# Kernel optimization log

Measured on AMD Instinct MI355X. Metric: run time of the kernel, lower is better.

## Reference

```python
import jax, jax.numpy as jnp
import numpy as np

NUM_STAB = 0.001  # numerical_stabilizer from relu_kernel_transformation


def relu_kernel(data, proj):
    """ReLU random-feature kernel: data [B,L,H,D], proj [M,D] -> [B,L,H,M]."""
    ratio = 1.0 / jnp.sqrt(jnp.asarray(proj.shape[0], jnp.float32))
    data_dash = ratio * jnp.einsum('blhd,md->blhm', data, proj)
    return jax.nn.relu(data_dash) + NUM_STAB


def setup_inputs() -> dict:
    key = jax.random.key(0)
    k1, k2, k3, k4 = jax.random.split(key, 4)
    B, L, H, D, M = 2, 4096, 8, 64, 256
    return {
        'query': jax.random.normal(k1, (B, L, H, D), jnp.float32),
        'key_t': jax.random.normal(k2, (B, L, H, D), jnp.float32),
        'value': jax.random.normal(k3, (B, L, H, D), jnp.float32),
        'projection_matrix': jax.random.normal(k4, (M, D), jnp.float32),
    }


def reference(query, key_t, value, projection_matrix):
    # Kernel feature maps [B,L,H,M]
    qp = relu_kernel(query, projection_matrix)
    kp = relu_kernel(key_t, projection_matrix)
    # Causal path operates in [L,B,H,*] layout
    qs = jnp.transpose(qp, (1, 0, 2, 3))     # [L,B,H,M]
    ks = jnp.transpose(kp, (1, 0, 2, 3))     # [L,B,H,M]
    vs = jnp.transpose(value, (1, 0, 2, 3))  # [L,B,H,D]

    B, H, M = qs.shape[1], qs.shape[2], qs.shape[3]
    D = vs.shape[3]
    init = (jnp.zeros((B, H, M, D), qs.dtype),  # running sum of k outer v
            jnp.zeros((B, H, M), qs.dtype))     # running sum of k

    def step(carry, inp):
        kv_sum, k_sum = carry
        q, k, v = inp  # [B,H,M], [B,H,M], [B,H,D]
        kv_sum = kv_sum + k[..., None] * v[..., None, :]
        k_sum = k_sum + k
        num = jnp.einsum('bhmd,bhm->bhd', kv_sum, q)  # causal numerator step
        den = jnp.einsum('bhm,bhm->bh', q, k_sum)     # causal denominator step
        return (kv_sum, k_sum), (num, den)

    _, (num, den) = jax.lax.scan(step, init, (qs, ks, vs))  # num [L,B,H,D], den [L,B,H]
    den = den[..., None]
    den = jnp.where(den <= 0.0, jnp.ones_like(den), den)
    out = num / den                      # [L,B,H,D]
    return jnp.transpose(out, (1, 0, 2, 3))  # [B,L,H,D]
```

## Files before the change

kernel.cpp:

```cpp
#include <hip/hip_runtime.h>
#include <hip/hip_bf16.h>


#define B_   2
#define L_   4096
#define H_   8
#define D_   64
#define M_   256
#define T_   128
#define C_   (L_ / T_)
#define NBH  (B_ * H_)
#define RATIO 0.0625f
#define STAB  0.001f
#define SVT  136
#define SQS  72

typedef __attribute__((ext_vector_type(8))) short short8;
typedef __attribute__((ext_vector_type(4))) float floatx4;

#define MFMA16(a, b, c) __builtin_amdgcn_mfma_f32_16x16x32_bf16(a, b, c, 0, 0, 0)

__device__ inline unsigned short f2bf(float x) {
    union { float f; unsigned u; } v; v.f = x;
    unsigned r = v.u + 0x7FFF + ((v.u >> 16) & 1);
    return (unsigned short)(r >> 16);
}
__device__ inline unsigned pack2bf(float a, float b) {
    __hip_bfloat162 h = __float22bfloat162_rn(make_float2(a, b));
    unsigned u; __builtin_memcpy(&u, &h, 4);
    return u;
}
__device__ inline short8 ldg8_bfs(const float* p) {
    float4 a = *(const float4*)p;
    float4 b = *(const float4*)(p + 4);
    short8 r;
    r[0] = (short)f2bf(a.x * RATIO); r[1] = (short)f2bf(a.y * RATIO);
    r[2] = (short)f2bf(a.z * RATIO); r[3] = (short)f2bf(a.w * RATIO);
    r[4] = (short)f2bf(b.x * RATIO); r[5] = (short)f2bf(b.y * RATIO);
    r[6] = (short)f2bf(b.z * RATIO); r[7] = (short)f2bf(b.w * RATIO);
    return r;
}

__global__ __launch_bounds__(256, 2)
void prep_kernel(const float* __restrict__ key, const float* __restrict__ val,
                 const float* __restrict__ proj,
                 unsigned short* __restrict__ kbf, unsigned short* __restrict__ VTg,
                 unsigned short* __restrict__ Pbf) {
    const int c = blockIdx.x, bh = blockIdx.y;
    const int b = bh / H_, h = bh % H_;
    const int tid = threadIdx.x;
    __shared__ __align__(16) unsigned short VT[64 * SVT];

    const size_t rowstr = H_ * D_;
    const size_t base = ((size_t)b * L_ + (size_t)c * T_) * rowstr + (size_t)h * D_;

    for (int i = tid; i < T_ * 16; i += 256) {
        int t = i >> 4, dd = (i & 15) * 4;
        float4 kv = *(const float4*)(key + base + (size_t)t * rowstr + dd);
        uint2 o; o.x = pack2bf(kv.x * RATIO, kv.y * RATIO);
        o.y = pack2bf(kv.z * RATIO, kv.w * RATIO);
        *(uint2*)(kbf + base + (size_t)t * rowstr + dd) = o;
    }
    for (int i = tid; i < T_ * 16; i += 256) {
        int t = i >> 4, d4 = (i & 15) * 4;
        float4 vv = *(const float4*)(val + base + (size_t)t * rowstr + d4);
        VT[(d4 + 0) * SVT + t] = f2bf(vv.x);
        VT[(d4 + 1) * SVT + t] = f2bf(vv.y);
        VT[(d4 + 2) * SVT + t] = f2bf(vv.z);
        VT[(d4 + 3) * SVT + t] = f2bf(vv.w);
    }
    __syncthreads();
    unsigned short* vout = VTg + ((size_t)bh * C_ + c) * (D_ * T_);
    for (int i = tid; i < D_ * 16; i += 256) {
        int d = i >> 4, tt = (i & 15) * 8;
        *(uint4*)(vout + d * T_ + tt) = *(const uint4*)&VT[d * SVT + tt];
    }
    if (c == 0) {
        int i = bh * 256 + tid;
        float4 pv = *(const float4*)(proj + (size_t)i * 4);
        uint2 o; o.x = pack2bf(pv.x, pv.y); o.y = pack2bf(pv.z, pv.w);
        *(uint2*)(Pbf + (size_t)i * 4) = o;
    }
}

__global__ __launch_bounds__(256, 2)
void scan_kernel(const unsigned short* __restrict__ kbf,
                 const unsigned short* __restrict__ VTg,
                 const unsigned short* __restrict__ Pbf,
                 unsigned short* __restrict__ S, float* __restrict__ Z) {
    const int mq = blockIdx.x, bh = blockIdx.y, dh = blockIdx.z;
    const int b = bh / H_, h = bh % H_;
    const int tid = threadIdx.x;
    const int w = tid >> 6, lane = tid & 63;
    const int l15 = lane & 15, quad = lane >> 4;
    const int dt = w & 1, ct2 = w >> 1;

    __shared__ __align__(16) unsigned short KpT[2][32 * SVT];
    __shared__ float zP[2][4][32];

    const size_t rowstr = H_ * D_;

    short8 pf[2][2];
#pragma unroll
    for (int ct = 0; ct < 2; ++ct)
#pragma unroll
        for (int kk = 0; kk < 2; ++kk)
            pf[ct][kk] = *(const short8*)(Pbf + (size_t)(mq * 32 + ct * 16 + l15) * D_
                                          + kk * 32 + quad * 8);

    floatx4 acc = {0.f, 0.f, 0.f, 0.f};
    float zreg = 0.f;

    short8 kf[2][2];
#pragma unroll
    for (int rt = 0; rt < 2; ++rt)
#pragma unroll
        for (int kk = 0; kk < 2; ++kk)
            kf[rt][kk] = *(const short8*)(kbf + ((size_t)b * L_) * rowstr + (size_t)h * D_
                                          + (size_t)(32 * w + rt * 16 + l15) * rowstr
                                          + kk * 32 + quad * 8);

    const int vrow = dh * 32 + dt * 16 + l15;
    const int drow0 = dh * 32 + dt * 16 + quad * 4;
    const int mcol = mq * 32 + ct2 * 16 + l15;

    for (int c = 0; c < C_; ++c) {
        const int buf = c & 1;
        float zpart[2] = {0.f, 0.f};
#pragma unroll
        for (int rt = 0; rt < 2; ++rt)
#pragma unroll
            for (int ct = 0; ct < 2; ++ct) {
                floatx4 a = {0.f, 0.f, 0.f, 0.f};
                a = MFMA16(kf[rt][0], pf[ct][0], a);
                a = MFMA16(kf[rt][1], pf[ct][1], a);
                float k0 = fmaxf(a[0], 0.f) + STAB;
                float k1 = fmaxf(a[1], 0.f) + STAB;
                float k2 = fmaxf(a[2], 0.f) + STAB;
                float k3 = fmaxf(a[3], 0.f) + STAB;
                zpart[ct] += (k0 + k1) + (k2 + k3);
                uint2 pk; pk.x = pack2bf(k0, k1); pk.y = pack2bf(k2, k3);
                *(uint2*)&KpT[buf][(ct * 16 + l15) * SVT + 32 * w + rt * 16 + quad * 4] = pk;
            }
#pragma unroll
        for (int ct = 0; ct < 2; ++ct) {
            float z = zpart[ct];
            z += __shfl_xor(z, 16, 64);
            z += __shfl_xor(z, 32, 64);
            if (quad == 0) zP[buf][w][ct * 16 + l15] = z;
        }
        if (c + 1 < C_) {
            const size_t kb2 = ((size_t)b * L_ + (size_t)(c + 1) * T_) * rowstr + (size_t)h * D_;
#pragma unroll
            for (int rt = 0; rt < 2; ++rt)
#pragma unroll
                for (int kk = 0; kk < 2; ++kk)
                    kf[rt][kk] = *(const short8*)(kbf + kb2
                                                  + (size_t)(32 * w + rt * 16 + l15) * rowstr
                                                  + kk * 32 + quad * 8);
        }
        const unsigned short* vbase = VTg + ((size_t)bh * C_ + c) * (D_ * T_);
        short8 vf[4];
#pragma unroll
        for (int k4 = 0; k4 < 4; ++k4)
            vf[k4] = *(const short8*)(vbase + (size_t)vrow * T_ + k4 * 32 + quad * 8);

        __syncthreads();

        unsigned short* Sp = S + ((size_t)bh * C_ + c) * (M_ * D_);
#pragma unroll
        for (int r = 0; r < 4; ++r)
            Sp[(size_t)(drow0 + r) * M_ + mcol] = f2bf(acc[r]);
        if (dh == 0 && w == 0 && lane < 32) {
            float zs = zP[buf][0][lane] + zP[buf][1][lane]
                     + zP[buf][2][lane] + zP[buf][3][lane];
            Z[((size_t)bh * C_ + c) * M_ + mq * 32 + lane] = zreg;
            zreg += zs;
        }
#pragma unroll
        for (int k4 = 0; k4 < 4; ++k4) {
            short8 kb = *(const short8*)&KpT[buf][(ct2 * 16 + l15) * SVT + k4 * 32 + quad * 8];
            acc = MFMA16(vf[k4], kb, acc);
        }
    }
}

__global__ __launch_bounds__(512, 2)
void phase3_kernel(const float* __restrict__ q,
                   const unsigned short* __restrict__ kbf,
                   const unsigned short* __restrict__ VTg,
                   const unsigned short* __restrict__ Pbf,
                   const unsigned short* __restrict__ S, const float* __restrict__ Z,
                   float* __restrict__ out) {
    const int c = blockIdx.x, bh = blockIdx.y;
    const int b = bh / H_, h = bh % H_;
    const int tid = threadIdx.x;
    const int w = tid >> 6, lane = tid & 63;
    const int l15 = lane & 15, quad = lane >> 4;

    __shared__ __align__(16) unsigned short KpL[T_ * SVT];
    __shared__ __align__(16) unsigned short QpS[8 * 16 * SQS];

    const size_t rowstr = H_ * D_;
    const size_t base = ((size_t)b * L_ + (size_t)c * T_) * rowstr + (size_t)h * D_;
    const unsigned short* Sp = S + (size_t)(bh * C_ + c) * (M_ * D_);
    const float* Zp = Z + (size_t)(bh * C_ + c) * M_;
    const unsigned short* Vc = VTg + ((size_t)bh * C_ + c) * (D_ * T_);

    short8 qf[2], kf[2];
#pragma unroll
    for (int kk = 0; kk < 2; ++kk) {
        size_t ro = base + (size_t)(16 * w + l15) * rowstr + kk * 32 + quad * 8;
        qf[kk] = ldg8_bfs(q + ro);
        kf[kk] = *(const short8*)(kbf + ro);
    }

    unsigned short* myQp = QpS + w * 16 * SQS;
    floatx4 num[4];
    floatx4 Aacc[8];
#pragma unroll
    for (int dt = 0; dt < 4; ++dt) { floatx4 z4 = {0.f,0.f,0.f,0.f}; num[dt] = z4; }
#pragma unroll
    for (int ct = 0; ct < 8; ++ct) { floatx4 z4 = {0.f,0.f,0.f,0.f}; Aacc[ct] = z4; }
    float dz[4] = {0.f, 0.f, 0.f, 0.f};

    for (int hh = 0; hh < 2; ++hh) {
        short8 qa[4];
#pragma unroll
        for (int fgl = 0; fgl < 2; ++fgl) {
            const int fg = 2 * hh + fgl;
#pragma unroll
            for (int ct = 0; ct < 4; ++ct) {
                const unsigned short* pp = Pbf + (size_t)(fg * 64 + ct * 16 + l15) * D_;
                short8 pf0 = *(const short8*)(pp + quad * 8);
                short8 pf1 = *(const short8*)(pp + 32 + quad * 8);
                floatx4 aq = {0.f, 0.f, 0.f, 0.f};
                aq = MFMA16(qf[0], pf0, aq);
                aq = MFMA16(qf[1], pf1, aq);
                floatx4 ak = {0.f, 0.f, 0.f, 0.f};
                ak = MFMA16(kf[0], pf0, ak);
                ak = MFMA16(kf[1], pf1, ak);
                const int mloc = fgl * 64 + ct * 16 + l15;
                float zv = Zp[hh * 128 + mloc];
#pragma unroll
                for (int r = 0; r < 4; ++r) {
                    float qpv = fmaxf(aq[r], 0.f) + STAB;
                    float kpv = fmaxf(ak[r], 0.f) + STAB;
                    myQp[(quad * 4 + r) * SQS + ct * 16 + l15] = f2bf(qpv);
                    KpL[(size_t)(16 * w + quad * 4 + r) * SVT + mloc] = f2bf(kpv);
                    dz[r] = fmaf(qpv, zv, dz[r]);
                }
            }
#pragma unroll
            for (int kk = 0; kk < 2; ++kk)
                qa[fgl * 2 + kk] = *(const short8*)&myQp[l15 * SQS + kk * 32 + quad * 8];
        }
#pragma unroll
        for (int dt = 0; dt < 4; ++dt)
#pragma unroll
            for (int kc = 0; kc < 4; ++kc) {
                short8 sb = *(const short8*)(Sp + (size_t)(dt * 16 + l15) * M_
                                             + hh * 128 + kc * 32 + quad * 8);
                num[dt] = MFMA16(qa[kc], sb, num[dt]);
            }
        __syncthreads();
#pragma unroll
        for (int ct = 0; ct < 8; ++ct) {
            if (ct <= w) {
#pragma unroll
                for (int kc = 0; kc < 4; ++kc) {
                    short8 kb = *(const short8*)&KpL[(size_t)(ct * 16 + l15) * SVT
                                                     + kc * 32 + quad * 8];
                    Aacc[ct] = MFMA16(qa[kc], kb, Aacc[ct]);
                }
            }
        }
        __syncthreads();
    }
#pragma unroll
    for (int r = 0; r < 4; ++r) {
        dz[r] += __shfl_xor(dz[r], 1, 64);
        dz[r] += __shfl_xor(dz[r], 2, 64);
        dz[r] += __shfl_xor(dz[r], 4, 64);
        dz[r] += __shfl_xor(dz[r], 8, 64);
    }

    unsigned short* AmL = KpL;
    float da[4] = {0.f, 0.f, 0.f, 0.f};
#pragma unroll
    for (int ct = 0; ct < 8; ++ct)
#pragma unroll
        for (int r = 0; r < 4; ++r) {
            float av = Aacc[ct][r];
            if (ct > w || (ct == w && l15 > quad * 4 + r)) av = 0.f;
            AmL[(size_t)(16 * w + quad * 4 + r) * SVT + ct * 16 + l15] = f2bf(av);
            da[r] += av;
        }
#pragma unroll
    for (int r = 0; r < 4; ++r) {
        da[r] += __shfl_xor(da[r], 1, 64);
        da[r] += __shfl_xor(da[r], 2, 64);
        da[r] += __shfl_xor(da[r], 4, 64);
        da[r] += __shfl_xor(da[r], 8, 64);
    }

    for (int k4 = 0; k4 <= (w >> 1); ++k4) {
        short8 am = *(const short8*)&AmL[(size_t)(16 * w + l15) * SVT
                                         + k4 * 32 + quad * 8];
#pragma unroll
        for (int dt = 0; dt < 4; ++dt) {
            short8 vb = *(const short8*)(Vc + (size_t)(dt * 16 + l15) * T_
                                         + k4 * 32 + quad * 8);
            num[dt] = MFMA16(am, vb, num[dt]);
        }
    }

#pragma unroll
    for (int r = 0; r < 4; ++r) {
        float den = da[r] + dz[r];
        if (den <= 0.f) den = 1.f;
        float inv = 1.f / den;
        int t = 16 * w + quad * 4 + r;
#pragma unroll
        for (int dt = 0; dt < 4; ++dt)
            out[base + (size_t)t * rowstr + dt * 16 + l15] = num[dt][r] * inv;
    }
}

extern "C" void kernel_launch(void* const* d_in, const int* in_sizes, int n_in,
                              void* d_out, int out_size, void* d_ws, size_t ws_size,
                              hipStream_t stream) {
    const float* q    = (const float*)d_in[0];
    const float* k    = (const float*)d_in[1];
    const float* v    = (const float*)d_in[2];
    const float* proj = (const float*)d_in[3];
    float* out = (float*)d_out;

    const size_t nS = (size_t)NBH * C_ * D_ * M_;
    const size_t nZ = (size_t)NBH * C_ * M_;
    const size_t nK = (size_t)B_ * L_ * H_ * D_;
    const size_t nV = (size_t)NBH * C_ * D_ * T_;
    unsigned short* S   = (unsigned short*)d_ws;
    float*          Z   = (float*)(S + nS);
    unsigned short* kbf = (unsigned short*)(Z + nZ);
    unsigned short* VTg = kbf + nK;
    unsigned short* Pbf = VTg + nV;

    prep_kernel<<<dim3(C_, NBH), dim3(256), 0, stream>>>(k, v, proj, kbf, VTg, Pbf);
    scan_kernel<<<dim3(8, NBH, 2), dim3(256), 0, stream>>>(kbf, VTg, Pbf, S, Z);
    phase3_kernel<<<dim3(C_, NBH), dim3(512), 0, stream>>>(q, kbf, VTg, Pbf, S, Z, out);
}
```

Measured before the change: 196.2 us.

## Warp-specialize scan kernel into producer/consumer waves and drop key bf16 precast

The scan kernel now runs 512 threads. Four producer waves compute the ReLU feature tile for the next chunk into a double-buffered LDS slot, while four consumer waves run the state-update MFMAs and store the S/Z prefix states for the current chunk. V fragments are prefetched one chunk ahead. The key bf16 conversion pass in prep_kernel is removed, and scan and phase3 now read fp32 keys and convert inline. This saves one workspace round-trip but doubles the key bytes each consumer reads, and it lowers occupancy to one block per CU.

```diff
diff --git a/kernel.cpp b/kernel.cpp
--- a/kernel.cpp
+++ b/kernel.cpp
@@ -42,10 +42,8 @@
 }
 
 __global__ __launch_bounds__(256, 2)
-void prep_kernel(const float* __restrict__ key, const float* __restrict__ val,
-                 const float* __restrict__ proj,
-                 unsigned short* __restrict__ kbf, unsigned short* __restrict__ VTg,
-                 unsigned short* __restrict__ Pbf) {
+void prep_kernel(const float* __restrict__ val, const float* __restrict__ proj,
+                 unsigned short* __restrict__ VTg, unsigned short* __restrict__ Pbf) {
     const int c = blockIdx.x, bh = blockIdx.y;
     const int b = bh / H_, h = bh % H_;
     const int tid = threadIdx.x;
@@ -54,13 +52,6 @@
     const size_t rowstr = H_ * D_;
     const size_t base = ((size_t)b * L_ + (size_t)c * T_) * rowstr + (size_t)h * D_;
 
-    for (int i = tid; i < T_ * 16; i += 256) {
-        int t = i >> 4, dd = (i & 15) * 4;
-        float4 kv = *(const float4*)(key + base + (size_t)t * rowstr + dd);
-        uint2 o; o.x = pack2bf(kv.x * RATIO, kv.y * RATIO);
-        o.y = pack2bf(kv.z * RATIO, kv.w * RATIO);
-        *(uint2*)(kbf + base + (size_t)t * rowstr + dd) = o;
-    }
     for (int i = tid; i < T_ * 16; i += 256) {
         int t = i >> 4, d4 = (i & 15) * 4;
         float4 vv = *(const float4*)(val + base + (size_t)t * rowstr + d4);
@@ -83,8 +74,8 @@
     }
 }
 
-__global__ __launch_bounds__(256, 2)
-void scan_kernel(const unsigned short* __restrict__ kbf,
+__global__ __launch_bounds__(512, 1)
+void scan_kernel(const float* __restrict__ key,
                  const unsigned short* __restrict__ VTg,
                  const unsigned short* __restrict__ Pbf,
                  unsigned short* __restrict__ S, float* __restrict__ Z) {
@@ -93,44 +84,34 @@
     const int tid = threadIdx.x;
     const int w = tid >> 6, lane = tid & 63;
     const int l15 = lane & 15, quad = lane >> 4;
-    const int dt = w & 1, ct2 = w >> 1;
 
     __shared__ __align__(16) unsigned short KpT[2][32 * SVT];
     __shared__ float zP[2][4][32];
 
     const size_t rowstr = H_ * D_;
-
-    short8 pf[2][2];
-#pragma unroll
-    for (int ct = 0; ct < 2; ++ct)
-#pragma unroll
-        for (int kk = 0; kk < 2; ++kk)
-            pf[ct][kk] = *(const short8*)(Pbf + (size_t)(mq * 32 + ct * 16 + l15) * D_
-                                          + kk * 32 + quad * 8);
-
-    floatx4 acc = {0.f, 0.f, 0.f, 0.f};
-    float zreg = 0.f;
-
-    short8 kf[2][2];
-#pragma unroll
-    for (int rt = 0; rt < 2; ++rt)
-#pragma unroll
-        for (int kk = 0; kk < 2; ++kk)
-            kf[rt][kk] = *(const short8*)(kbf + ((size_t)b * L_) * rowstr + (size_t)h * D_
-                                          + (size_t)(32 * w + rt * 16 + l15) * rowstr
-                                          + kk * 32 + quad * 8);
-
-    const int vrow = dh * 32 + dt * 16 + l15;
-    const int drow0 = dh * 32 + dt * 16 + quad * 4;
-    const int mcol = mq * 32 + ct2 * 16 + l15;
-
-    for (int c = 0; c < C_; ++c) {
-        const int buf = c & 1;
-        float zpart[2] = {0.f, 0.f};
+    const size_t khead = (size_t)b * L_ * rowstr + (size_t)h * D_;
+
+    if (w < 4) {
+        short8 pf[2][2];
+#pragma unroll
+        for (int ct = 0; ct < 2; ++ct)
+#pragma unroll
+            for (int kk = 0; kk < 2; ++kk)
+                pf[ct][kk] = *(const short8*)(Pbf + (size_t)(mq * 32 + ct * 16 + l15) * D_
+                                              + kk * 32 + quad * 8);
+        short8 kf[2][2];
 #pragma unroll
         for (int rt = 0; rt < 2; ++rt)
 #pragma unroll
-            for (int ct = 0; ct < 2; ++ct) {
+            for (int kk = 0; kk < 2; ++kk)
+                kf[rt][kk] = ldg8_bfs(key + khead
+                                      + (size_t)(32 * w + rt * 16 + l15) * rowstr
+                                      + kk * 32 + quad * 8);
+#pragma unroll
+        for (int ct = 0; ct < 2; ++ct) {
+            float zpart = 0.f;
+#pragma unroll
+            for (int rt = 0; rt < 2; ++rt) {
                 floatx4 a = {0.f, 0.f, 0.f, 0.f};
                 a = MFMA16(kf[rt][0], pf[ct][0], a);
                 a = MFMA16(kf[rt][1], pf[ct][1], a);
@@ -138,56 +119,110 @@
                 float k1 = fmaxf(a[1], 0.f) + STAB;
                 float k2 = fmaxf(a[2], 0.f) + STAB;
                 float k3 = fmaxf(a[3], 0.f) + STAB;
-                zpart[ct] += (k0 + k1) + (k2 + k3);
+                zpart += (k0 + k1) + (k2 + k3);
                 uint2 pk; pk.x = pack2bf(k0, k1); pk.y = pack2bf(k2, k3);
-                *(uint2*)&KpT[buf][(ct * 16 + l15) * SVT + 32 * w + rt * 16 + quad * 4] = pk;
-            }
-#pragma unroll
-        for (int ct = 0; ct < 2; ++ct) {
-            float z = zpart[ct];
-            z += __shfl_xor(z, 16, 64);
-            z += __shfl_xor(z, 32, 64);
-            if (quad == 0) zP[buf][w][ct * 16 + l15] = z;
-        }
-        if (c + 1 < C_) {
-            const size_t kb2 = ((size_t)b * L_ + (size_t)(c + 1) * T_) * rowstr + (size_t)h * D_;
-#pragma unroll
-            for (int rt = 0; rt < 2; ++rt)
-#pragma unroll
-                for (int kk = 0; kk < 2; ++kk)
-                    kf[rt][kk] = *(const short8*)(kbf + kb2
+                *(uint2*)&KpT[0][(ct * 16 + l15) * SVT + 32 * w + rt * 16 + quad * 4] = pk;
+            }
+            zpart += __shfl_xor(zpart, 16, 64);
+            zpart += __shfl_xor(zpart, 32, 64);
+            if (quad == 0) zP[0][w][ct * 16 + l15] = zpart;
+        }
+#pragma unroll
+        for (int rt = 0; rt < 2; ++rt)
+#pragma unroll
+            for (int kk = 0; kk < 2; ++kk)
+                kf[rt][kk] = ldg8_bfs(key + khead + (size_t)T_ * rowstr
+                                      + (size_t)(32 * w + rt * 16 + l15) * rowstr
+                                      + kk * 32 + quad * 8);
+        __syncthreads();
+        for (int c = 0; c < C_; ++c) {
+            const int buf = c & 1;
+            if (c + 1 < C_) {
+#pragma unroll
+                for (int ct = 0; ct < 2; ++ct) {
+                    float zpart = 0.f;
+#pragma unroll
+                    for (int rt = 0; rt < 2; ++rt) {
+                        floatx4 a = {0.f, 0.f, 0.f, 0.f};
+                        a = MFMA16(kf[rt][0], pf[ct][0], a);
+                        a = MFMA16(kf[rt][1], pf[ct][1], a);
+                        float k0 = fmaxf(a[0], 0.f) + STAB;
+                        float k1 = fmaxf(a[1], 0.f) + STAB;
+                        float k2 = fmaxf(a[2], 0.f) + STAB;
+                        float k3 = fmaxf(a[3], 0.f) + STAB;
+                        zpart += (k0 + k1) + (k2 + k3);
+                        uint2 pk; pk.x = pack2bf(k0, k1); pk.y = pack2bf(k2, k3);
+                        *(uint2*)&KpT[buf ^ 1][(ct * 16 + l15) * SVT
+                                               + 32 * w + rt * 16 + quad * 4] = pk;
+                    }
+                    zpart += __shfl_xor(zpart, 16, 64);
+                    zpart += __shfl_xor(zpart, 32, 64);
+                    if (quad == 0) zP[buf ^ 1][w][ct * 16 + l15] = zpart;
+                }
+                if (c + 2 < C_) {
+                    const size_t kb2 = khead + (size_t)(c + 2) * T_ * rowstr;
+#pragma unroll
+                    for (int rt = 0; rt < 2; ++rt)
+#pragma unroll
+                        for (int kk = 0; kk < 2; ++kk)
+                            kf[rt][kk] = ldg8_bfs(key + kb2
                                                   + (size_t)(32 * w + rt * 16 + l15) * rowstr
                                                   + kk * 32 + quad * 8);
-        }
-        const unsigned short* vbase = VTg + ((size_t)bh * C_ + c) * (D_ * T_);
+                }
+            }
+            __syncthreads();
+        }
+    } else {
+        const int w4 = w - 4;
+        const int dt = w4 & 1, ct2 = w4 >> 1;
+        const int vrow = dh * 32 + dt * 16 + l15;
+        const int drow0 = dh * 32 + dt * 16 + quad * 4;
+        const int mcol = mq * 32 + ct2 * 16 + l15;
+        const unsigned short* vhead = VTg + (size_t)bh * C_ * (D_ * T_);
+
+        floatx4 acc = {0.f, 0.f, 0.f, 0.f};
+        float zreg = 0.f;
         short8 vf[4];
 #pragma unroll
         for (int k4 = 0; k4 < 4; ++k4)
-            vf[k4] = *(const short8*)(vbase + (size_t)vrow * T_ + k4 * 32 + quad * 8);
-
+            vf[k4] = *(const short8*)(vhead + (size_t)vrow * T_ + k4 * 32 + quad * 8);
         __syncthreads();
-
-        unsigned short* Sp = S + ((size_t)bh * C_ + c) * (M_ * D_);
-#pragma unroll
-        for (int r = 0; r < 4; ++r)
-            Sp[(size_t)(drow0 + r) * M_ + mcol] = f2bf(acc[r]);
-        if (dh == 0 && w == 0 && lane < 32) {
-            float zs = zP[buf][0][lane] + zP[buf][1][lane]
-                     + zP[buf][2][lane] + zP[buf][3][lane];
-            Z[((size_t)bh * C_ + c) * M_ + mq * 32 + lane] = zreg;
-            zreg += zs;
-        }
-#pragma unroll
-        for (int k4 = 0; k4 < 4; ++k4) {
-            short8 kb = *(const short8*)&KpT[buf][(ct2 * 16 + l15) * SVT + k4 * 32 + quad * 8];
-            acc = MFMA16(vf[k4], kb, acc);
+        for (int c = 0; c < C_; ++c) {
+            const int buf = c & 1;
+            unsigned short* Sp = S + ((size_t)bh * C_ + c) * (M_ * D_);
+#pragma unroll
+            for (int r = 0; r < 4; ++r)
+                Sp[(size_t)(drow0 + r) * M_ + mcol] = f2bf(acc[r]);
+            if (w == 4 && dh == 0 && lane < 32) {
+                float zs = zP[buf][0][lane] + zP[buf][1][lane]
+                         + zP[buf][2][lane] + zP[buf][3][lane];
+                Z[((size_t)bh * C_ + c) * M_ + mq * 32 + lane] = zreg;
+                zreg += zs;
+            }
+            short8 vn[4];
+            if (c + 1 < C_) {
+                const unsigned short* vb2 = vhead + (size_t)(c + 1) * (D_ * T_);
+#pragma unroll
+                for (int k4 = 0; k4 < 4; ++k4)
+                    vn[k4] = *(const short8*)(vb2 + (size_t)vrow * T_ + k4 * 32 + quad * 8);
+            }
+#pragma unroll
+            for (int k4 = 0; k4 < 4; ++k4) {
+                short8 kb = *(const short8*)&KpT[buf][(ct2 * 16 + l15) * SVT
+                                                      + k4 * 32 + quad * 8];
+                acc = MFMA16(vf[k4], kb, acc);
+            }
+            if (c + 1 < C_) {
+#pragma unroll
+                for (int k4 = 0; k4 < 4; ++k4) vf[k4] = vn[k4];
+            }
+            __syncthreads();
         }
     }
 }
 
 __global__ __launch_bounds__(512, 2)
-void phase3_kernel(const float* __restrict__ q,
-                   const unsigned short* __restrict__ kbf,
+void phase3_kernel(const float* __restrict__ q, const float* __restrict__ key,
                    const unsigned short* __restrict__ VTg,
                    const unsigned short* __restrict__ Pbf,
                    const unsigned short* __restrict__ S, const float* __restrict__ Z,
@@ -212,7 +247,7 @@
     for (int kk = 0; kk < 2; ++kk) {
         size_t ro = base + (size_t)(16 * w + l15) * rowstr + kk * 32 + quad * 8;
         qf[kk] = ldg8_bfs(q + ro);
-        kf[kk] = *(const short8*)(kbf + ro);
+        kf[kk] = ldg8_bfs(key + ro);
     }
 
     unsigned short* myQp = QpS + w * 16 * SQS;
@@ -338,15 +373,13 @@
 
     const size_t nS = (size_t)NBH * C_ * D_ * M_;
     const size_t nZ = (size_t)NBH * C_ * M_;
-    const size_t nK = (size_t)B_ * L_ * H_ * D_;
     const size_t nV = (size_t)NBH * C_ * D_ * T_;
     unsigned short* S   = (unsigned short*)d_ws;
     float*          Z   = (float*)(S + nS);
-    unsigned short* kbf = (unsigned short*)(Z + nZ);
-    unsigned short* VTg = kbf + nK;
+    unsigned short* VTg = (unsigned short*)(Z + nZ);
     unsigned short* Pbf = VTg + nV;
 
-    prep_kernel<<<dim3(C_, NBH), dim3(256), 0, stream>>>(k, v, proj, kbf, VTg, Pbf);
-    scan_kernel<<<dim3(8, NBH, 2), dim3(256), 0, stream>>>(kbf, VTg, Pbf, S, Z);
-    phase3_kernel<<<dim3(C_, NBH), dim3(512), 0, stream>>>(q, kbf, VTg, Pbf, S, Z, out);
-}
+    prep_kernel<<<dim3(C_, NBH), dim3(256), 0, stream>>>(v, proj, VTg, Pbf);
+    scan_kernel<<<dim3(8, NBH, 2), dim3(512), 0, stream>>>(k, VTg, Pbf, S, Z);
+    phase3_kernel<<<dim3(C_, NBH), dim3(512), 0, stream>>>(q, k, VTg, Pbf, S, Z, out);
+}
```

Result: faster. 184.0 us (-6.2%).
